# Performance work log

Measured on AMD Instinct MI355X. Metric: run time of the kernel, lower is better.

## Reference

```python
import jax, jax.numpy as jnp
import numpy as np

N_NODES = 50000
N_EDGES = 500000
NUM_ATOM_TYPES = 11
EMBED_DIM = 128
HID_DIM = 128
OUT_DIM = 64
NUM_GRAPHS = 512


def setup_inputs() -> dict:
    key = jax.random.key(0)
    ks = jax.random.split(key, 12)
    x = jax.random.randint(ks[0], (N_NODES,), 0, NUM_ATOM_TYPES, dtype=jnp.int64) if jax.config.jax_enable_x64 else jax.random.randint(ks[0], (N_NODES,), 0, NUM_ATOM_TYPES, dtype=jnp.int32)
    edge_index = jax.random.randint(ks[1], (2, N_EDGES), 0, N_NODES, dtype=jnp.int32)
    batch = jnp.sort(jax.random.randint(ks[2], (N_NODES,), 0, NUM_GRAPHS, dtype=jnp.int32))
    s = 0.05
    embed = jax.random.normal(ks[3], (NUM_ATOM_TYPES, EMBED_DIM), jnp.float32) * s
    W0 = jax.random.normal(ks[4], (EMBED_DIM, HID_DIM), jnp.float32) * s
    b0 = jnp.zeros((HID_DIM,), jnp.float32)
    W1 = jax.random.normal(ks[5], (HID_DIM, HID_DIM), jnp.float32) * s
    b1 = jnp.zeros((HID_DIM,), jnp.float32)
    W2 = jax.random.normal(ks[6], (HID_DIM, HID_DIM), jnp.float32) * s
    b2 = jnp.zeros((HID_DIM,), jnp.float32)
    fc_w = jax.random.normal(ks[7], (HID_DIM, OUT_DIM), jnp.float32) * s
    fc_b = jnp.zeros((OUT_DIM,), jnp.float32)
    return {"x": x, "edge_index": edge_index, "batch": batch, "embed": embed,
            "W0": W0, "b0": b0, "W1": W1, "b1": b1, "W2": W2, "b2": b2,
            "fc_w": fc_w, "fc_b": fc_b}


def reference(x, edge_index, batch, embed, W0, b0, W1, b1, W2, b2, fc_w, fc_b):
    N = x.shape[0]
    src, dst = edge_index[0], edge_index[1]
    # GCN symmetric normalization with self-loops: deg counts incoming edges + self-loop
    deg = jax.ops.segment_sum(jnp.ones((src.shape[0],), jnp.float32), dst, num_segments=N) + 1.0
    dinv = jax.lax.rsqrt(deg)                     # [N]
    enorm = dinv[src] * dinv[dst]                 # [E] edge norm
    self_norm = dinv * dinv                       # [N] self-loop norm
    h = embed[x]                                  # [N, embed_dim]
    for W, b in ((W0, b0), (W1, b1), (W2, b2)):
        h = h @ W                                 # transform then propagate (PyG GCNConv)
        agg = jax.ops.segment_sum(h[src] * enorm[:, None], dst, num_segments=N)
        h = jax.nn.relu(agg + h * self_norm[:, None] + b)
        # dropout is identity in eval mode
    counts = jax.ops.segment_sum(jnp.ones((N,), jnp.float32), batch, num_segments=NUM_GRAPHS)
    pooled = jax.ops.segment_sum(h, batch, num_segments=NUM_GRAPHS) / jnp.maximum(counts, 1.0)[:, None]
    return pooled @ fc_w + fc_b                   # [NUM_GRAPHS, out_dim]
```

## Files before the change

kernel.cpp:

```cpp
#include <hip/hip_runtime.h>

#define NN 50000
#define NE 500000
#define NT 11
#define D  128
#define OD 64
#define NG 512
#define SLOTS 40
#define EB 1954
#define PB 196

typedef __attribute__((ext_vector_type(8))) short short8;
typedef __attribute__((ext_vector_type(4))) float f32x4;

static __device__ __forceinline__ unsigned short f2b(float f) {
  unsigned u = __float_as_uint(f);
  return (unsigned short)((u + 0x7fffu + ((u >> 16) & 1u)) >> 16);
}
static __device__ __forceinline__ float b2f_lo(unsigned u) {
  return __uint_as_float(u << 16);
}
static __device__ __forceinline__ float b2f_hi(unsigned u) {
  return __uint_as_float(u & 0xffff0000u);
}
static __device__ __forceinline__ unsigned pack2(float lo, float hi) {
  return (unsigned)f2b(lo) | ((unsigned)f2b(hi) << 16);
}

__global__ void k_fillprep(const int* __restrict__ src, const int* __restrict__ dst,
                           const int* __restrict__ x, int* __restrict__ cur,
                           int2* __restrict__ slots,
                           const float* __restrict__ embed, const float* __restrict__ W0,
                           const float* __restrict__ W1, const float* __restrict__ W2,
                           const int* __restrict__ batch, float* __restrict__ EW,
                           unsigned short* __restrict__ WT1, unsigned short* __restrict__ WT2,
                           int* __restrict__ gs) {
  if (blockIdx.x < EB) {
    int e = blockIdx.x * 256 + threadIdx.x;
    if (e < NE) {
      int s = src[e], d = dst[e];
      int pos = atomicAdd(&cur[d], 1);
      if (pos < SLOTS) slots[d * SLOTS + pos] = make_int2(s, x[s]);
    }
    return;
  }
  int gt = (blockIdx.x - EB) * 256 + threadIdx.x;
  const int NTH = PB * 256;
  for (int idx = gt; idx < 2 * D * D; idx += NTH) {
    const float* W = (idx < D * D) ? W1 : W2;
    unsigned short* WT = (idx < D * D) ? WT1 : WT2;
    int i = idx & (D * D - 1);
    int k = i >> 7, c = i & 127;
    WT[c * D + k] = f2b(W[k * D + c]);
  }
  for (int idx = gt; idx < NT * D; idx += NTH) {
    int r = idx >> 7, c = idx & 127;
    float acc = 0.f;
    for (int k = 0; k < D; ++k) acc += embed[r * D + k] * W0[k * D + c];
    EW[idx] = acc;
  }
  for (int i = gt; i < NN; i += NTH) {
    int b = batch[i];
    if (i == 0) { for (int g = 0; g <= b; ++g) gs[g] = 0; }
    else { int bp = batch[i - 1]; for (int g = bp + 1; g <= b; ++g) gs[g] = i; }
    if (i == NN - 1) { for (int g = b + 1; g <= NG; ++g) gs[g] = NN; }
  }
}

__launch_bounds__(256)
__global__ void k_agg0(const float* __restrict__ EW, const int* __restrict__ x,
                       const int* __restrict__ cur, unsigned* __restrict__ hs,
                       const int2* __restrict__ slots, const float* __restrict__ b) {
  __shared__ float sEW[NT * D];
  int tid = threadIdx.x;
  for (int i = tid; i < NT * D; i += 256) sEW[i] = EW[i];
  __syncthreads();
  int n = __builtin_amdgcn_readfirstlane(blockIdx.x * 4 + (tid >> 6));
  int lane = tid & 63;
  int degn = cur[n];
  float dn = rsqrtf((float)degn + 1.0f);
  int deg = degn < SLOTS ? degn : SLOTS;
  const int2* sl = slots + (size_t)n * SLOTS;
  float2 sv = ((const float2*)(sEW + x[n] * D))[lane];
  float ax = sv.x * dn, ay = sv.y * dn;
  float a0x = 0.f, a0y = 0.f, a1x = 0.f, a1y = 0.f;
  float a2x = 0.f, a2y = 0.f, a3x = 0.f, a3y = 0.f;
  int e = 0;
  for (; e + 3 < deg; e += 4) {
    int2 p0 = sl[e], p1 = sl[e + 1], p2 = sl[e + 2], p3 = sl[e + 3];
    float w0 = rsqrtf((float)cur[p0.x] + 1.0f);
    float w1 = rsqrtf((float)cur[p1.x] + 1.0f);
    float w2 = rsqrtf((float)cur[p2.x] + 1.0f);
    float w3 = rsqrtf((float)cur[p3.x] + 1.0f);
    float2 v0 = ((const float2*)(sEW + p0.y * D))[lane];
    float2 v1 = ((const float2*)(sEW + p1.y * D))[lane];
    float2 v2 = ((const float2*)(sEW + p2.y * D))[lane];
    float2 v3 = ((const float2*)(sEW + p3.y * D))[lane];
    a0x += v0.x * w0; a0y += v0.y * w0;
    a1x += v1.x * w1; a1y += v1.y * w1;
    a2x += v2.x * w2; a2y += v2.y * w2;
    a3x += v3.x * w3; a3y += v3.y * w3;
  }
  for (; e < deg; ++e) {
    int2 pp = sl[e];
    float w = rsqrtf((float)cur[pp.x] + 1.0f);
    float2 v = ((const float2*)(sEW + pp.y * D))[lane];
    ax += v.x * w; ay += v.y * w;
  }
  ax += (a0x + a1x) + (a2x + a3x);
  ay += (a0y + a1y) + (a2y + a3y);
  float2 bb = ((const float2*)b)[lane];
  float ox = fmaxf(ax * dn + bb.x, 0.f) * dn;
  float oy = fmaxf(ay * dn + bb.y, 0.f) * dn;
  hs[(size_t)n * (D / 2) + lane] = pack2(ox, oy);
}

template <int SCALE_OUT>
__launch_bounds__(256)
__global__ void k_conv(const unsigned* __restrict__ hs_in,
                       const unsigned short* __restrict__ WT,
                       const int* __restrict__ cur, const int2* __restrict__ slots,
                       const float* __restrict__ b, unsigned short* __restrict__ out) {
  __shared__ unsigned short Gt[16 * D];
  int tid = threadIdx.x;
  int wid = tid >> 6, lane = tid & 63;
  char* tile = (char*)Gt;
  int base = blockIdx.x * 16;

  for (int r = 0; r < 4; ++r) {
    int row = (wid << 2) + r;
    int n = __builtin_amdgcn_readfirstlane(base + row);
    int degn = cur[n];
    int deg = degn < SLOTS ? degn : SLOTS;
    const int2* sl = slots + (size_t)n * SLOTS;
    unsigned su = hs_in[(size_t)n * (D / 2) + lane];
    float ax = b2f_lo(su), ay = b2f_hi(su);
    float a0x = 0.f, a0y = 0.f, a1x = 0.f, a1y = 0.f;
    float a2x = 0.f, a2y = 0.f, a3x = 0.f, a3y = 0.f;
    float a4x = 0.f, a4y = 0.f, a5x = 0.f, a5y = 0.f;
    float a6x = 0.f, a6y = 0.f, a7x = 0.f, a7y = 0.f;
    int e = 0;
    for (; e + 7 < deg; e += 8) {
      int s0 = sl[e].x, s1 = sl[e + 1].x, s2 = sl[e + 2].x, s3 = sl[e + 3].x;
      int s4 = sl[e + 4].x, s5 = sl[e + 5].x, s6 = sl[e + 6].x, s7 = sl[e + 7].x;
      unsigned u0 = hs_in[(size_t)s0 * (D / 2) + lane];
      unsigned u1 = hs_in[(size_t)s1 * (D / 2) + lane];
      unsigned u2 = hs_in[(size_t)s2 * (D / 2) + lane];
      unsigned u3 = hs_in[(size_t)s3 * (D / 2) + lane];
      unsigned u4 = hs_in[(size_t)s4 * (D / 2) + lane];
      unsigned u5 = hs_in[(size_t)s5 * (D / 2) + lane];
      unsigned u6 = hs_in[(size_t)s6 * (D / 2) + lane];
      unsigned u7 = hs_in[(size_t)s7 * (D / 2) + lane];
      a0x += b2f_lo(u0); a0y += b2f_hi(u0);
      a1x += b2f_lo(u1); a1y += b2f_hi(u1);
      a2x += b2f_lo(u2); a2y += b2f_hi(u2);
      a3x += b2f_lo(u3); a3y += b2f_hi(u3);
      a4x += b2f_lo(u4); a4y += b2f_hi(u4);
      a5x += b2f_lo(u5); a5y += b2f_hi(u5);
      a6x += b2f_lo(u6); a6y += b2f_hi(u6);
      a7x += b2f_lo(u7); a7y += b2f_hi(u7);
    }
    for (; e + 3 < deg; e += 4) {
      int s0 = sl[e].x, s1 = sl[e + 1].x, s2 = sl[e + 2].x, s3 = sl[e + 3].x;
      unsigned u0 = hs_in[(size_t)s0 * (D / 2) + lane];
      unsigned u1 = hs_in[(size_t)s1 * (D / 2) + lane];
      unsigned u2 = hs_in[(size_t)s2 * (D / 2) + lane];
      unsigned u3 = hs_in[(size_t)s3 * (D / 2) + lane];
      a0x += b2f_lo(u0); a0y += b2f_hi(u0);
      a1x += b2f_lo(u1); a1y += b2f_hi(u1);
      a2x += b2f_lo(u2); a2y += b2f_hi(u2);
      a3x += b2f_lo(u3); a3y += b2f_hi(u3);
    }
    for (; e < deg; ++e) {
      unsigned u = hs_in[(size_t)sl[e].x * (D / 2) + lane];
      ax += b2f_lo(u); ay += b2f_hi(u);
    }
    ax += ((a0x + a1x) + (a2x + a3x)) + ((a4x + a5x) + (a6x + a7x));
    ay += ((a0y + a1y) + (a2y + a3y)) + ((a4y + a5y) + (a6y + a7y));
    int ba = (row << 8) + ((lane << 2) ^ ((row & 7) << 4));
    *(unsigned*)(tile + ba) = pack2(ax, ay);
  }
  __syncthreads();

  int l15 = lane & 15, l4 = lane >> 4;
  f32x4 acc[2];
  acc[0] = (f32x4){0.f, 0.f, 0.f, 0.f};
  acc[1] = (f32x4){0.f, 0.f, 0.f, 0.f};
#pragma unroll
  for (int ks = 0; ks < 4; ++ks) {
    int k0 = (ks << 6) | (l4 << 4);
    int ba = (l15 << 8) + (k0 ^ ((l15 & 7) << 4));
    short8 a = *(const short8*)(tile + ba);
#pragma unroll
    for (int c = 0; c < 2; ++c) {
      int ct = (wid << 1) + c;
      short8 bfr = *(const short8*)(WT + ((ct << 4) + l15) * D + ks * 32 + (l4 << 3));
      acc[c] = __builtin_amdgcn_mfma_f32_16x16x32_bf16(a, bfr, acc[c], 0, 0, 0);
    }
  }

#pragma unroll
  for (int c = 0; c < 2; ++c) {
    int ct = (wid << 1) + c;
    float bb = b[(ct << 4) + l15];
#pragma unroll
    for (int r = 0; r < 4; ++r) {
      int n2 = base + (l4 << 2) + r;
      float dv = rsqrtf((float)cur[n2] + 1.0f);
      float v = fmaxf(acc[c][r] * dv + bb, 0.f);
      if (SCALE_OUT) v *= dv;
      out[(size_t)n2 * D + (ct << 4) + l15] = f2b(v);
    }
  }
}

__launch_bounds__(64)
__global__ void k_pool(const unsigned* __restrict__ h, const int* __restrict__ gs,
                       const float* __restrict__ fw, const float* __restrict__ fb,
                       float* __restrict__ out) {
  __shared__ float p[D];
  int g = blockIdx.x, lane = threadIdx.x;
  int s = gs[g], e = gs[g + 1];
  float px = 0.f, py = 0.f;
  for (int n = s; n < e; ++n) {
    unsigned u = h[(size_t)n * (D / 2) + lane];
    px += b2f_lo(u); py += b2f_hi(u);
  }
  int cnt = e - s;
  float inv = 1.f / (float)(cnt > 0 ? cnt : 1);
  p[lane * 2] = px * inv;
  p[lane * 2 + 1] = py * inv;
  __syncthreads();
  float o = fb[lane];
  for (int k = 0; k < D; ++k) o += p[k] * fw[k * OD + lane];
  out[g * OD + lane] = o;
}

extern "C" void kernel_launch(void* const* d_in, const int* in_sizes, int n_in,
                              void* d_out, int out_size, void* d_ws, size_t ws_size,
                              hipStream_t stream) {
  const int* x     = (const int*)d_in[0];
  const int* ei    = (const int*)d_in[1];
  const int* batch = (const int*)d_in[2];
  const float* embed = (const float*)d_in[3];
  const float* W0  = (const float*)d_in[4];
  const float* b0  = (const float*)d_in[5];
  const float* W1  = (const float*)d_in[6];
  const float* b1  = (const float*)d_in[7];
  const float* W2  = (const float*)d_in[8];
  const float* b2  = (const float*)d_in[9];
  const float* fw  = (const float*)d_in[10];
  const float* fb  = (const float*)d_in[11];
  float* out = (float*)d_out;
  const int* src = ei;
  const int* dst = ei + NE;

  char* p = (char*)d_ws;
  auto alloc = [&](size_t bytes) {
    char* r = p;
    p += (bytes + 255) & ~(size_t)255;
    return r;
  };
  unsigned* bufA = (unsigned*)alloc((size_t)NN * D * 2);
  unsigned* bufB = (unsigned*)alloc((size_t)NN * D * 2);
  int*  cur   = (int*)alloc((size_t)NN * 4);
  int2* slots = (int2*)alloc((size_t)NN * SLOTS * 8);
  float* EW   = (float*)alloc((size_t)NT * D * 4);
  unsigned short* WT1 = (unsigned short*)alloc((size_t)D * D * 2);
  unsigned short* WT2 = (unsigned short*)alloc((size_t)D * D * 2);
  int*  gs    = (int*)alloc((size_t)(NG + 1) * 4);

  hipMemsetAsync(cur, 0, (size_t)NN * 4, stream);
  k_fillprep<<<EB + PB, 256, 0, stream>>>(src, dst, x, cur, slots,
                                          embed, W0, W1, W2, batch, EW, WT1, WT2, gs);
  k_agg0<<<NN / 4, 256, 0, stream>>>(EW, x, cur, bufA, slots, b0);
  k_conv<1><<<NN / 16, 256, 0, stream>>>(bufA, WT1, cur, slots, b1, (unsigned short*)bufB);
  k_conv<0><<<NN / 16, 256, 0, stream>>>(bufB, WT2, cur, slots, b2, (unsigned short*)bufA);
  k_pool<<<NG, 64, 0, stream>>>(bufA, gs, fw, fb, out);
}
```

Before: 179.6 us.

## Fuse mean-pool into last GCN layer and shrink edge slots to int

The final conv layer now accumulates its ReLU outputs into per-graph pooled sums in shared memory and global atomics, instead of writing bf16 node features and re-reading them in a separate pool kernel. The pool kernel becomes a small FC-only kernel that divides by node counts. Edge slots now store only the source index (int instead of int2), so the slot array is half the size. In exchange, the first layer looks up x[s] per neighbour, and the pooled sums use float atomics whose summation order is nondeterministic.

```diff
diff --git a/kernel.cpp b/kernel.cpp
--- a/kernel.cpp
+++ b/kernel.cpp
@@ -28,8 +28,7 @@
 }
 
 __global__ void k_fillprep(const int* __restrict__ src, const int* __restrict__ dst,
-                           const int* __restrict__ x, int* __restrict__ cur,
-                           int2* __restrict__ slots,
+                           int* __restrict__ cur, int* __restrict__ slots,
                            const float* __restrict__ embed, const float* __restrict__ W0,
                            const float* __restrict__ W1, const float* __restrict__ W2,
                            const int* __restrict__ batch, float* __restrict__ EW,
@@ -40,7 +39,7 @@
     if (e < NE) {
       int s = src[e], d = dst[e];
       int pos = atomicAdd(&cur[d], 1);
-      if (pos < SLOTS) slots[d * SLOTS + pos] = make_int2(s, x[s]);
+      if (pos < SLOTS) slots[d * SLOTS + pos] = s;
     }
     return;
   }
@@ -70,7 +69,7 @@
 __launch_bounds__(256)
 __global__ void k_agg0(const float* __restrict__ EW, const int* __restrict__ x,
                        const int* __restrict__ cur, unsigned* __restrict__ hs,
-                       const int2* __restrict__ slots, const float* __restrict__ b) {
+                       const int* __restrict__ slots, const float* __restrict__ b) {
   __shared__ float sEW[NT * D];
   int tid = threadIdx.x;
   for (int i = tid; i < NT * D; i += 256) sEW[i] = EW[i];
@@ -80,31 +79,31 @@
   int degn = cur[n];
   float dn = rsqrtf((float)degn + 1.0f);
   int deg = degn < SLOTS ? degn : SLOTS;
-  const int2* sl = slots + (size_t)n * SLOTS;
+  const int* sl = slots + (size_t)n * SLOTS;
   float2 sv = ((const float2*)(sEW + x[n] * D))[lane];
   float ax = sv.x * dn, ay = sv.y * dn;
   float a0x = 0.f, a0y = 0.f, a1x = 0.f, a1y = 0.f;
   float a2x = 0.f, a2y = 0.f, a3x = 0.f, a3y = 0.f;
   int e = 0;
   for (; e + 3 < deg; e += 4) {
-    int2 p0 = sl[e], p1 = sl[e + 1], p2 = sl[e + 2], p3 = sl[e + 3];
-    float w0 = rsqrtf((float)cur[p0.x] + 1.0f);
-    float w1 = rsqrtf((float)cur[p1.x] + 1.0f);
-    float w2 = rsqrtf((float)cur[p2.x] + 1.0f);
-    float w3 = rsqrtf((float)cur[p3.x] + 1.0f);
-    float2 v0 = ((const float2*)(sEW + p0.y * D))[lane];
-    float2 v1 = ((const float2*)(sEW + p1.y * D))[lane];
-    float2 v2 = ((const float2*)(sEW + p2.y * D))[lane];
-    float2 v3 = ((const float2*)(sEW + p3.y * D))[lane];
+    int s0 = sl[e], s1 = sl[e + 1], s2 = sl[e + 2], s3 = sl[e + 3];
+    float w0 = rsqrtf((float)cur[s0] + 1.0f);
+    float w1 = rsqrtf((float)cur[s1] + 1.0f);
+    float w2 = rsqrtf((float)cur[s2] + 1.0f);
+    float w3 = rsqrtf((float)cur[s3] + 1.0f);
+    float2 v0 = ((const float2*)(sEW + x[s0] * D))[lane];
+    float2 v1 = ((const float2*)(sEW + x[s1] * D))[lane];
+    float2 v2 = ((const float2*)(sEW + x[s2] * D))[lane];
+    float2 v3 = ((const float2*)(sEW + x[s3] * D))[lane];
     a0x += v0.x * w0; a0y += v0.y * w0;
     a1x += v1.x * w1; a1y += v1.y * w1;
     a2x += v2.x * w2; a2y += v2.y * w2;
     a3x += v3.x * w3; a3y += v3.y * w3;
   }
   for (; e < deg; ++e) {
-    int2 pp = sl[e];
-    float w = rsqrtf((float)cur[pp.x] + 1.0f);
-    float2 v = ((const float2*)(sEW + pp.y * D))[lane];
+    int s = sl[e];
+    float w = rsqrtf((float)cur[s] + 1.0f);
+    float2 v = ((const float2*)(sEW + x[s] * D))[lane];
     ax += v.x * w; ay += v.y * w;
   }
   ax += (a0x + a1x) + (a2x + a3x);
@@ -115,13 +114,15 @@
   hs[(size_t)n * (D / 2) + lane] = pack2(ox, oy);
 }
 
-template <int SCALE_OUT>
+template <int FUSE_POOL>
 __launch_bounds__(256)
 __global__ void k_conv(const unsigned* __restrict__ hs_in,
                        const unsigned short* __restrict__ WT,
-                       const int* __restrict__ cur, const int2* __restrict__ slots,
-                       const float* __restrict__ b, unsigned short* __restrict__ out) {
+                       const int* __restrict__ cur, const int* __restrict__ slots,
+                       const float* __restrict__ b, unsigned short* __restrict__ out,
+                       const int* __restrict__ batch, float* __restrict__ pooled) {
   __shared__ unsigned short Gt[16 * D];
+  __shared__ float Ot[FUSE_POOL ? 16 * D : 1];
   int tid = threadIdx.x;
   int wid = tid >> 6, lane = tid & 63;
   char* tile = (char*)Gt;
@@ -132,7 +133,7 @@
     int n = __builtin_amdgcn_readfirstlane(base + row);
     int degn = cur[n];
     int deg = degn < SLOTS ? degn : SLOTS;
-    const int2* sl = slots + (size_t)n * SLOTS;
+    const int* sl = slots + (size_t)n * SLOTS;
     unsigned su = hs_in[(size_t)n * (D / 2) + lane];
     float ax = b2f_lo(su), ay = b2f_hi(su);
     float a0x = 0.f, a0y = 0.f, a1x = 0.f, a1y = 0.f;
@@ -141,8 +142,8 @@
     float a6x = 0.f, a6y = 0.f, a7x = 0.f, a7y = 0.f;
     int e = 0;
     for (; e + 7 < deg; e += 8) {
-      int s0 = sl[e].x, s1 = sl[e + 1].x, s2 = sl[e + 2].x, s3 = sl[e + 3].x;
-      int s4 = sl[e + 4].x, s5 = sl[e + 5].x, s6 = sl[e + 6].x, s7 = sl[e + 7].x;
+      int s0 = sl[e], s1 = sl[e + 1], s2 = sl[e + 2], s3 = sl[e + 3];
+      int s4 = sl[e + 4], s5 = sl[e + 5], s6 = sl[e + 6], s7 = sl[e + 7];
       unsigned u0 = hs_in[(size_t)s0 * (D / 2) + lane];
       unsigned u1 = hs_in[(size_t)s1 * (D / 2) + lane];
       unsigned u2 = hs_in[(size_t)s2 * (D / 2) + lane];
@@ -161,7 +162,7 @@
       a7x += b2f_lo(u7); a7y += b2f_hi(u7);
     }
     for (; e + 3 < deg; e += 4) {
-      int s0 = sl[e].x, s1 = sl[e + 1].x, s2 = sl[e + 2].x, s3 = sl[e + 3].x;
+      int s0 = sl[e], s1 = sl[e + 1], s2 = sl[e + 2], s3 = sl[e + 3];
       unsigned u0 = hs_in[(size_t)s0 * (D / 2) + lane];
       unsigned u1 = hs_in[(size_t)s1 * (D / 2) + lane];
       unsigned u2 = hs_in[(size_t)s2 * (D / 2) + lane];
@@ -172,7 +173,7 @@
       a3x += b2f_lo(u3); a3y += b2f_hi(u3);
     }
     for (; e < deg; ++e) {
-      unsigned u = hs_in[(size_t)sl[e].x * (D / 2) + lane];
+      unsigned u = hs_in[(size_t)sl[e] * (D / 2) + lane];
       ax += b2f_lo(u); ay += b2f_hi(u);
     }
     ax += ((a0x + a1x) + (a2x + a3x)) + ((a4x + a5x) + (a6x + a7x));
@@ -208,28 +209,39 @@
       int n2 = base + (l4 << 2) + r;
       float dv = rsqrtf((float)cur[n2] + 1.0f);
       float v = fmaxf(acc[c][r] * dv + bb, 0.f);
-      if (SCALE_OUT) v *= dv;
-      out[(size_t)n2 * D + (ct << 4) + l15] = f2b(v);
-    }
+      if (FUSE_POOL) {
+        Ot[((l4 << 2) + r) * D + (ct << 4) + l15] = v;
+      } else {
+        out[(size_t)n2 * D + (ct << 4) + l15] = f2b(v * dv);
+      }
+    }
+  }
+  if (FUSE_POOL) {
+    __syncthreads();
+    int col = tid & 127, part = tid >> 7;
+    int r0 = part * 8;
+    int gprev = batch[base + r0];
+    float sum = 0.f;
+#pragma unroll
+    for (int r = 0; r < 8; ++r) {
+      int g = batch[base + r0 + r];
+      if (g != gprev) { atomicAdd(&pooled[gprev * D + col], sum); sum = 0.f; gprev = g; }
+      sum += Ot[(r0 + r) * D + col];
+    }
+    atomicAdd(&pooled[gprev * D + col], sum);
   }
 }
 
 __launch_bounds__(64)
-__global__ void k_pool(const unsigned* __restrict__ h, const int* __restrict__ gs,
-                       const float* __restrict__ fw, const float* __restrict__ fb,
-                       float* __restrict__ out) {
+__global__ void k_fc(const float* __restrict__ pooled, const int* __restrict__ gs,
+                     const float* __restrict__ fw, const float* __restrict__ fb,
+                     float* __restrict__ out) {
   __shared__ float p[D];
   int g = blockIdx.x, lane = threadIdx.x;
-  int s = gs[g], e = gs[g + 1];
-  float px = 0.f, py = 0.f;
-  for (int n = s; n < e; ++n) {
-    unsigned u = h[(size_t)n * (D / 2) + lane];
-    px += b2f_lo(u); py += b2f_hi(u);
-  }
-  int cnt = e - s;
+  int cnt = gs[g + 1] - gs[g];
   float inv = 1.f / (float)(cnt > 0 ? cnt : 1);
-  p[lane * 2] = px * inv;
-  p[lane * 2 + 1] = py * inv;
+  p[lane] = pooled[g * D + lane] * inv;
+  p[lane + 64] = pooled[g * D + lane + 64] * inv;
   __syncthreads();
   float o = fb[lane];
   for (int k = 0; k < D; ++k) o += p[k] * fw[k * OD + lane];
@@ -263,18 +275,21 @@
   };
   unsigned* bufA = (unsigned*)alloc((size_t)NN * D * 2);
   unsigned* bufB = (unsigned*)alloc((size_t)NN * D * 2);
-  int*  cur   = (int*)alloc((size_t)NN * 4);
-  int2* slots = (int2*)alloc((size_t)NN * SLOTS * 8);
-  float* EW   = (float*)alloc((size_t)NT * D * 4);
+  int*   cur    = (int*)alloc((size_t)NN * 4);
+  float* pooled = (float*)alloc((size_t)NG * D * 4);
+  int*   slots  = (int*)alloc((size_t)NN * SLOTS * 4);
+  float* EW     = (float*)alloc((size_t)NT * D * 4);
   unsigned short* WT1 = (unsigned short*)alloc((size_t)D * D * 2);
   unsigned short* WT2 = (unsigned short*)alloc((size_t)D * D * 2);
-  int*  gs    = (int*)alloc((size_t)(NG + 1) * 4);
-
-  hipMemsetAsync(cur, 0, (size_t)NN * 4, stream);
-  k_fillprep<<<EB + PB, 256, 0, stream>>>(src, dst, x, cur, slots,
+  int*   gs     = (int*)alloc((size_t)(NG + 1) * 4);
+
+  hipMemsetAsync(cur, 0, (size_t)((char*)pooled - (char*)cur) + (size_t)NG * D * 4, stream);
+  k_fillprep<<<EB + PB, 256, 0, stream>>>(src, dst, cur, slots,
                                           embed, W0, W1, W2, batch, EW, WT1, WT2, gs);
   k_agg0<<<NN / 4, 256, 0, stream>>>(EW, x, cur, bufA, slots, b0);
-  k_conv<1><<<NN / 16, 256, 0, stream>>>(bufA, WT1, cur, slots, b1, (unsigned short*)bufB);
-  k_conv<0><<<NN / 16, 256, 0, stream>>>(bufB, WT2, cur, slots, b2, (unsigned short*)bufA);
-  k_pool<<<NG, 64, 0, stream>>>(bufA, gs, fw, fb, out);
-}
+  k_conv<0><<<NN / 16, 256, 0, stream>>>(bufA, WT1, cur, slots, b1,
+                                         (unsigned short*)bufB, batch, pooled);
+  k_conv<1><<<NN / 16, 256, 0, stream>>>(bufB, WT2, cur, slots, b2,
+                                         nullptr, batch, pooled);
+  k_fc<<<NG, 64, 0, stream>>>(pooled, gs, fw, fb, out);
+}
```

Result: faster. 147.2 us (-18.0%).
